# Performance work log

Measured on AMD Instinct MI355X. Metric: run time of the kernel, lower is better.

Reference implementation:

```python
import jax, jax.numpy as jnp
import numpy as np

NFE = 8            # round(time / step_size) = round(1.0 / 0.125)
STEP = 0.125


def setup_inputs() -> dict:
    key = jax.random.key(0)
    k1, k2, k3 = jax.random.split(key, 3)
    N, C, V, L = 64, 64, 500, 12
    x = jax.random.normal(k1, (N, C, V, L), dtype=jnp.float32)
    # random adjacency, row-normalized (typical diffusion operator; keeps Euler stable)
    adj = jax.random.uniform(k2, (V, V), dtype=jnp.float32)
    adj = adj / jnp.sum(adj, axis=1, keepdims=True)
    in_total = (NFE + 1) * C  # 576
    out_dim = 64
    W = jax.random.normal(k3, (out_dim, in_total), dtype=jnp.float32) * (1.0 / np.sqrt(in_total))
    b = jnp.zeros((out_dim,), dtype=jnp.float32)
    return {"x": x, "adj": adj, "W": W, "b": b}


def reference(x, adj, W, b):
    # Euler integration of dx/dt = A x over the node dim:
    # out[n,c,v,l] = sum_w x[n,c,w,l] * A[v,w]
    states = [x]
    cur = x
    for _ in range(NFE):  # fixed, small step count
        ax = jnp.einsum('ncwl,vw->ncvl', cur, adj)
        cur = cur + STEP * ax
        states.append(cur)
    h = jnp.concatenate(states, axis=1)  # [N, (NFE+1)*C, V, L]
    # 1x1 Conv2d == channel GEMM
    out = jnp.einsum('ncvl,oc->novl', h, W) + b[None, :, None, None]
    return out
```

## Files before the change

kernel.cpp:

```cpp
#include <hip/hip_runtime.h>
#include <hip/hip_bf16.h>
#include <stdint.h>

typedef __attribute__((ext_vector_type(8))) short short8;
typedef __attribute__((ext_vector_type(4))) short short4v;
typedef __attribute__((ext_vector_type(4))) float f32x4;
typedef __attribute__((ext_vector_type(4))) float fvec4;

__device__ __forceinline__ short f2bf(float f) {
  unsigned u = __builtin_bit_cast(unsigned, f);
  unsigned r = u + 0x7fffu + ((u >> 16) & 1u);
  return (short)(r >> 16);
}

__device__ __forceinline__ void gload_lds16(const void* g, void* l) {
  __builtin_amdgcn_global_load_lds(
      (const __attribute__((address_space(1))) void*)g,
      (__attribute__((address_space(3))) void*)l, 16, 0, 0);
}

#define VP   512
#define TILE_SHORTS 8192
#define PANEL_TILES 72
#define NSTEP 66

__device__ __forceinline__ int tswz(int r, int c) {
  return r * 64 + ((((c >> 3) ^ (r & 7)) << 3) | (c & 7));
}

__global__ __launch_bounds__(256) void initM_kernel(const float* __restrict__ adj,
    float* __restrict__ Mpow, short* __restrict__ Mt, short* __restrict__ M1T) {
  int idx = blockIdx.x * 256 + threadIdx.x;
  int v = idx >> 9, w = idx & 511;
  float m = 0.f;
  if (v < 500 && w < 500) m = 0.125f * adj[v * 500 + w] + (v == w ? 1.f : 0.f);
  Mpow[idx] = m;
  M1T[(size_t)w * VP + v] = f2bf(m);
  int bx = v >> 7, r = v & 127, c = w & 63;
  int kt0 = (w >> 6), kt1 = 8 + (w >> 6);
  Mt[(size_t)(bx * PANEL_TILES + kt0) * TILE_SHORTS + tswz(r, c)] =
      f2bf((v == w && v < 500) ? 1.f : 0.f);
  Mt[(size_t)(bx * PANEL_TILES + kt1) * TILE_SHORTS + tswz(r, c)] = f2bf(m);
}

__global__ __launch_bounds__(256) void powstep_kernel(const float* __restrict__ src,
    const short* __restrict__ M1T, float* __restrict__ dst,
    short* __restrict__ Mt, int kslice) {
  int tid = threadIdx.x, wv = tid >> 6, lane = tid & 63;
  int tile = blockIdx.x * 4 + wv;
  int tv = tile >> 5, tw = tile & 31;
  int row  = tv * 16 + (lane & 15);
  int colw = tw * 16 + (lane & 15);
  int kgrp = (lane >> 4) * 8;
  const short* mcol = M1T + (size_t)colw * VP;
  f32x4 acc = {0.f, 0.f, 0.f, 0.f};
  for (int k0 = 0; k0 < 512; k0 += 32) {
    int kc = k0 + kgrp;
    fvec4 f0 = *(const fvec4*)&src[row * VP + kc];
    fvec4 f1 = *(const fvec4*)&src[row * VP + kc + 4];
    short8 a;
    for (int t = 0; t < 4; ++t) { a[t] = f2bf(f0[t]); a[4 + t] = f2bf(f1[t]); }
    short8 b = *(const short8*)&mcol[kc];
    acc = __builtin_amdgcn_mfma_f32_16x16x32_bf16(a, b, acc, 0, 0, 0);
  }
  for (int r = 0; r < 4; ++r) {
    int i = (lane >> 4) * 4 + r;
    int vv = tv * 16 + i;
    float val = acc[r];
    dst[vv * VP + colw] = val;
    int bx = vv >> 7, rr = vv & 127, c = colw & 63;
    int kt = kslice * 8 + (colw >> 6);
    Mt[(size_t)(bx * PANEL_TILES + kt) * TILE_SHORTS + tswz(rr, c)] = f2bf(val);
  }
}

__global__ __launch_bounds__(256) void xpose_kernel(const float* __restrict__ x,
    short* __restrict__ xb) {
  int t = threadIdx.x, wv = t >> 6, lane = t & 63;
  int p  = blockIdx.x & 1;
  int w0 = (blockIdx.x >> 1) * 64;
  int n  = blockIdx.y;
  const float* xs = x + (size_t)n * 64 * 6000;
  __shared__ short xl[32 * 770];
  for (int ci = 0; ci < 8; ++ci) {
    int crow = wv * 8 + ci;
    int c = p * 32 + crow;
    for (int i = 0; i < 3; ++i) {
      int wl = (i * 64 + lane) * 4;
      int gwl = w0 * 12 + wl;
      fvec4 v = {0.f, 0.f, 0.f, 0.f};
      if (gwl + 3 < 6000) {
        v = *(const fvec4*)&xs[(size_t)c * 6000 + gwl];
      } else {
        for (int e = 0; e < 4; ++e)
          if (gwl + e < 6000) v[e] = xs[(size_t)c * 6000 + gwl + e];
      }
      for (int e = 0; e < 4; ++e) xl[crow * 770 + wl + e] = f2bf(v[e]);
    }
  }
  __syncthreads();
  for (int i = 0; i < 12; ++i) {
    int ct = i * 256 + t;
    int bl = ct & 3;
    int w_l = (ct >> 2) & 63;
    int l = ct >> 8;
    short8 s;
    for (int j = 0; j < 8; ++j)
      s[j] = xl[(bl * 8 + j) * 770 + w_l * 12 + l];
    size_t dst = ((size_t)(n * 12 + l) * 512 + w0 + w_l) * 64 + (p * 4 + bl) * 8;
    *(short8*)(xb + dst) = s;
  }
}

__global__ __launch_bounds__(256) void zbuild_kernel(const short* __restrict__ xb,
    const float* __restrict__ W, short* __restrict__ Zt, int n0) {
  int t = threadIdx.x, wv = t >> 6, lane = t & 63;
  int lh = blockIdx.x;
  int l = lh >> 1, wh = lh & 1;
  int nloc = blockIdx.y;
  int n = n0 + nloc;
  const short* xbase = xb + (size_t)(n * 12 + l) * 512 * 64;
  short8 af[4][2];
  for (int q = 0; q < 4; ++q)
    for (int ks = 0; ks < 2; ++ks) {
      int wrow = wh * 256 + wv * 64 + q * 16 + (lane & 15);
      int cblk = ks * 4 + (lane >> 4);
      af[q][ks] = *(const short8*)(xbase + (size_t)wrow * 64 + cblk * 8);
    }
  int lanebase = (lane & 15) * 12 + l;
  int kt_off = wh * 4 + wv;
  for (int j = 0; j < 36; ++j) {
    int k = j >> 2;
    int o = (j & 3) * 16 + (lane & 15);
    const float* wp = W + o * 576 + k * 64;
    short8 bw[2];
    for (int ks = 0; ks < 2; ++ks) {
      fvec4 f0 = *(const fvec4*)(wp + ks * 32 + (lane >> 4) * 8);
      fvec4 f1 = *(const fvec4*)(wp + ks * 32 + (lane >> 4) * 8 + 4);
      for (int e = 0; e < 4; ++e) { bw[ks][e] = f2bf(f0[e]); bw[ks][4 + e] = f2bf(f1[e]); }
    }
    f32x4 acc[4];
    for (int q = 0; q < 4; ++q) {
      acc[q] = (f32x4){0.f, 0.f, 0.f, 0.f};
      acc[q] = __builtin_amdgcn_mfma_f32_16x16x32_bf16(af[q][0], bw[0], acc[q], 0, 0, 0);
      acc[q] = __builtin_amdgcn_mfma_f32_16x16x32_bf16(af[q][1], bw[1], acc[q], 0, 0, 0);
    }
    int zr = (j & 3) * 192 + lanebase;
    int pr = zr >> 7, rr = zr & 127;
    size_t tbase = ((size_t)(nloc * 6 + pr) * PANEL_TILES + k * 8 + kt_off) * TILE_SHORTS
                 + rr * 64;
    for (int q = 0; q < 4; ++q) {
      int c4 = q * 16 + (lane >> 4) * 4;
      size_t idx = tbase + ((((c4 >> 3) ^ (zr & 7)) << 3) | (c4 & 7));
      short4v s;
      for (int e = 0; e < 4; ++e) s[e] = f2bf(acc[q][e]);
      *(short4v*)(Zt + idx) = s;
    }
  }
}

__global__ __launch_bounds__(256) void biggemm_kernel(const short* __restrict__ Zt,
    const short* __restrict__ Mt, const float* __restrict__ bvec,
    float* __restrict__ out, int n0) {
  int tid = threadIdx.x, wv = tid >> 6, lane = tid & 63;
  int nwg = gridDim.x;
  int b = blockIdx.x;
  int swz = (b & 7) * (nwg >> 3) + (b >> 3);
  int bx = swz & 3;
  int rest = swz >> 2;
  int by = rest % 6;
  int bz = rest / 6;
  int v0    = bx * 128;
  int rowM0 = by * 128;
  int n = n0 + bz;
  __shared__ short As[2][TILE_SHORTS];
  __shared__ short Bs[2][TILE_SHORTS];
  f32x4 acc[4][4];
  for (int i = 0; i < 4; ++i)
    for (int j = 0; j < 4; ++j) acc[i][j] = (f32x4){0.f, 0.f, 0.f, 0.f};
  int wr = wv >> 1, wc = wv & 1;
  const char* Apanel = (const char*)(Zt + (size_t)(bz * 6 + by) * PANEL_TILES * TILE_SHORTS);
  const char* Bpanel = (const char*)(Mt + (size_t)bx * PANEL_TILES * TILE_SHORTS);

  auto ktmap = [&](int s) { return (s < 2) ? (bx * 2 + s) : (s + 6); };

  auto STAGE = [&](int p, int kt) {
    const char* a  = Apanel + (size_t)kt * (TILE_SHORTS * 2);
    const char* bb = Bpanel + (size_t)kt * (TILE_SHORTS * 2);
#pragma unroll
    for (int cc = 0; cc < 4; ++cc) {
      int chunk = cc * 4 + wv;
      int off = chunk * 1024 + lane * 16;
      gload_lds16(a + off,  (char*)As[p] + chunk * 1024);
      gload_lds16(bb + off, (char*)Bs[p] + chunk * 1024);
    }
  };

  STAGE(0, ktmap(0));
  STAGE(1, ktmap(1));

  for (int s = 0; s < NSTEP; ++s) {
    int d = s & 1;
    if (s < NSTEP - 1) {
      asm volatile("s_waitcnt vmcnt(8)" ::: "memory");
    } else {
      asm volatile("s_waitcnt vmcnt(0)" ::: "memory");
    }
    __builtin_amdgcn_sched_barrier(0);
    __builtin_amdgcn_s_barrier();

    short8 af[2][4], bf[2][4];
#pragma unroll
    for (int kk = 0; kk < 2; ++kk) {
      int cbyte = kk * 64 + (lane >> 4) * 16;
#pragma unroll
      for (int mi = 0; mi < 4; ++mi) {
        int r = wr * 64 + mi * 16 + (lane & 15);
        af[kk][mi] = *(const short8*)((const char*)As[d] + r * 128 + (cbyte ^ ((r & 7) << 4)));
      }
#pragma unroll
      for (int ni = 0; ni < 4; ++ni) {
        int r = wc * 64 + ni * 16 + (lane & 15);
        bf[kk][ni] = *(const short8*)((const char*)Bs[d] + r * 128 + (cbyte ^ ((r & 7) << 4)));
      }
    }
    asm volatile("s_waitcnt lgkmcnt(0)" ::: "memory");
    __builtin_amdgcn_sched_barrier(0);
    __builtin_amdgcn_s_barrier();

    if (s + 2 < NSTEP) STAGE(d, ktmap(s + 2));

    __builtin_amdgcn_s_setprio(1);
#pragma unroll
    for (int kk = 0; kk < 2; ++kk)
#pragma unroll
      for (int mi = 0; mi < 4; ++mi)
#pragma unroll
        for (int ni = 0; ni < 4; ++ni)
          acc[mi][ni] = __builtin_amdgcn_mfma_f32_16x16x32_bf16(af[kk][mi], bf[kk][ni],
                                                                acc[mi][ni], 0, 0, 0);
    __builtin_amdgcn_s_setprio(0);
  }

  for (int mi = 0; mi < 4; ++mi) {
    for (int r = 0; r < 4; ++r) {
      int gm = rowM0 + wr * 64 + mi * 16 + (lane >> 4) * 4 + r;
      int o = gm / 12, l = gm - o * 12;
      float bo = bvec[o];
      size_t obase = (((size_t)n * 64 + o) * 500) * 12 + l;
      for (int ni = 0; ni < 4; ++ni) {
        int v = v0 + wc * 64 + ni * 16 + (lane & 15);
        if (v < 500) out[obase + (size_t)v * 12] = acc[mi][ni][r] + bo;
      }
    }
  }
}

extern "C" void kernel_launch(void* const* d_in, const int* in_sizes, int n_in,
                              void* d_out, int out_size, void* d_ws, size_t ws_size,
                              hipStream_t stream) {
  const float* x   = (const float*)d_in[0];
  const float* adj = (const float*)d_in[1];
  const float* W   = (const float*)d_in[2];
  const float* bv  = (const float*)d_in[3];
  float* out = (float*)d_out;
  char* ws = (char*)d_ws;

  size_t off = 0;
  float* Mpow0 = (float*)(ws + off); off += (size_t)512 * 512 * 4;
  float* Mpow1 = (float*)(ws + off); off += (size_t)512 * 512 * 4;
  short* M1T   = (short*)(ws + off); off += (size_t)512 * 512 * 2;
  short* Mt    = (short*)(ws + off); off += (size_t)4 * PANEL_TILES * TILE_SHORTS * 2;
  short* xb    = (short*)(ws + off); off += (size_t)64 * 12 * 512 * 64 * 2;
  short* Zt    = (short*)(ws + off);
  size_t per_n = (size_t)6 * PANEL_TILES * TILE_SHORTS * 2;
  int nchunk = 1;
  if (ws_size > off) {
    size_t a = (ws_size - off) / per_n;
    nchunk = (a >= 16) ? 16 : (a < 1 ? 1 : (int)a);
  }

  hipLaunchKernelGGL(initM_kernel, dim3(1024), dim3(256), 0, stream, adj, Mpow0, Mt, M1T);
  const float* src = Mpow0; float* dst = Mpow1;
  for (int k = 2; k <= 8; ++k) {
    hipLaunchKernelGGL(powstep_kernel, dim3(256), dim3(256), 0, stream, src, M1T, dst, Mt, k);
    float* t = dst; dst = (float*)src; src = t;
  }
  hipLaunchKernelGGL(xpose_kernel, dim3(16, 64), dim3(256), 0, stream, x, xb);
  for (int n0 = 0; n0 < 64; n0 += nchunk) {
    int cn = (64 - n0) < nchunk ? (64 - n0) : nchunk;
    hipLaunchKernelGGL(zbuild_kernel, dim3(24, cn), dim3(256), 0, stream, xb, W, Zt, n0);
    hipLaunchKernelGGL(biggemm_kernel, dim3(24 * cn), dim3(256), 0, stream, Zt, Mt, bv, out, n0);
  }
}
```

Before: 584.3 us.

## Load GEMM B operand directly from global into registers, skipping LDS staging

The B fragments are now read straight from global memory into registers, double-buffered one k-step ahead, instead of being staged through LDS. Only the A tile still goes through LDS, and the vmcnt wait thresholds are adjusted to match. This halves LDS use and removes the B LDS writes and reads, which could allow more resident workgroups. In exchange, each wave issues its own global loads for B, so B data is duplicated across waves in the cache, and the two register buffers for B raise VGPR pressure.

```diff
diff --git a/kernel.cpp b/kernel.cpp
--- a/kernel.cpp
+++ b/kernel.cpp
@@ -174,7 +174,6 @@
   int rowM0 = by * 128;
   int n = n0 + bz;
   __shared__ short As[2][TILE_SHORTS];
-  __shared__ short Bs[2][TILE_SHORTS];
   f32x4 acc[4][4];
   for (int i = 0; i < 4; ++i)
     for (int j = 0; j < 4; ++j) acc[i][j] = (f32x4){0.f, 0.f, 0.f, 0.f};
@@ -184,32 +183,43 @@
 
   auto ktmap = [&](int s) { return (s < 2) ? (bx * 2 + s) : (s + 6); };
 
-  auto STAGE = [&](int p, int kt) {
-    const char* a  = Apanel + (size_t)kt * (TILE_SHORTS * 2);
-    const char* bb = Bpanel + (size_t)kt * (TILE_SHORTS * 2);
+  auto STAGE_A = [&](int p, int kt) {
+    const char* a = Apanel + (size_t)kt * (TILE_SHORTS * 2);
 #pragma unroll
     for (int cc = 0; cc < 4; ++cc) {
       int chunk = cc * 4 + wv;
       int off = chunk * 1024 + lane * 16;
-      gload_lds16(a + off,  (char*)As[p] + chunk * 1024);
-      gload_lds16(bb + off, (char*)Bs[p] + chunk * 1024);
+      gload_lds16(a + off, (char*)As[p] + chunk * 1024);
     }
   };
 
-  STAGE(0, ktmap(0));
-  STAGE(1, ktmap(1));
-
-  for (int s = 0; s < NSTEP; ++s) {
+  const char* Bgbase = Bpanel + (lane & 15) * 128 + wc * 8192;
+  int offk0 = (((lane >> 4) * 16)      ^ ((lane & 7) << 4));
+  int offk1 = ((64 + (lane >> 4) * 16) ^ ((lane & 7) << 4));
+  auto BLOAD = [&](int kt, short8 (&bfn)[2][4]) {
+    const char* p0 = Bgbase + (size_t)kt * (TILE_SHORTS * 2) + offk0;
+    const char* p1 = Bgbase + (size_t)kt * (TILE_SHORTS * 2) + offk1;
+#pragma unroll
+    for (int ni = 0; ni < 4; ++ni) {
+      bfn[0][ni] = *(const short8*)(p0 + ni * 2048);
+      bfn[1][ni] = *(const short8*)(p1 + ni * 2048);
+    }
+  };
+
+  short8 bfA[2][4], bfB[2][4];
+
+  auto STEP = [&](int s, short8 (&bfc)[2][4], short8 (&bfn)[2][4]) {
     int d = s & 1;
     if (s < NSTEP - 1) {
-      asm volatile("s_waitcnt vmcnt(8)" ::: "memory");
+      asm volatile("s_waitcnt vmcnt(4)" ::: "memory");
     } else {
       asm volatile("s_waitcnt vmcnt(0)" ::: "memory");
     }
     __builtin_amdgcn_sched_barrier(0);
     __builtin_amdgcn_s_barrier();
-
-    short8 af[2][4], bf[2][4];
+    if (s + 1 < NSTEP) BLOAD(ktmap(s + 1), bfn);
+    __builtin_amdgcn_sched_barrier(0);
+    short8 af[2][4];
 #pragma unroll
     for (int kk = 0; kk < 2; ++kk) {
       int cbyte = kk * 64 + (lane >> 4) * 16;
@@ -218,18 +228,11 @@
         int r = wr * 64 + mi * 16 + (lane & 15);
         af[kk][mi] = *(const short8*)((const char*)As[d] + r * 128 + (cbyte ^ ((r & 7) << 4)));
       }
-#pragma unroll
-      for (int ni = 0; ni < 4; ++ni) {
-        int r = wc * 64 + ni * 16 + (lane & 15);
-        bf[kk][ni] = *(const short8*)((const char*)Bs[d] + r * 128 + (cbyte ^ ((r & 7) << 4)));
-      }
     }
     asm volatile("s_waitcnt lgkmcnt(0)" ::: "memory");
     __builtin_amdgcn_sched_barrier(0);
     __builtin_amdgcn_s_barrier();
-
-    if (s + 2 < NSTEP) STAGE(d, ktmap(s + 2));
-
+    if (s + 2 < NSTEP) STAGE_A(d, ktmap(s + 2));
     __builtin_amdgcn_s_setprio(1);
 #pragma unroll
     for (int kk = 0; kk < 2; ++kk)
@@ -237,9 +240,18 @@
       for (int mi = 0; mi < 4; ++mi)
 #pragma unroll
         for (int ni = 0; ni < 4; ++ni)
-          acc[mi][ni] = __builtin_amdgcn_mfma_f32_16x16x32_bf16(af[kk][mi], bf[kk][ni],
+          acc[mi][ni] = __builtin_amdgcn_mfma_f32_16x16x32_bf16(af[kk][mi], bfc[kk][ni],
                                                                 acc[mi][ni], 0, 0, 0);
     __builtin_amdgcn_s_setprio(0);
+  };
+
+  STAGE_A(0, ktmap(0));
+  BLOAD(ktmap(0), bfA);
+  STAGE_A(1, ktmap(1));
+
+  for (int ss = 0; ss < NSTEP; ss += 2) {
+    STEP(ss,     bfA, bfB);
+    STEP(ss + 1, bfB, bfA);
   }
 
   for (int mi = 0; mi < 4; ++mi) {
```

Result: slower. 695.2 us (+19.0%).
